# Performance work log

Measured on AMD Instinct MI355X. Metric: run time of the kernel, lower is better.

The kernel has to match this reference:

```python
import jax, jax.numpy as jnp
import numpy as np

WS = 16      # window_size
OWS = 24     # overlap_win_size = int(16*0.5) + 16
PAD = 4      # (OWS - WS) // 2
NH = 6       # num_heads
DIM = 192
MLP_HID = 384  # dim * mlp_ratio(2)
TABLE = (WS + OWS - 1) ** 2  # 1521


def _ln(x, g, b, eps=1e-5):
    m = x.mean(-1, keepdims=True)
    v = ((x - m) ** 2).mean(-1, keepdims=True)
    return (x - m) * jax.lax.rsqrt(v + eps) * g + b


def setup_inputs() -> dict:
    key = jax.random.key(0)
    ks = jax.random.split(key, 16)
    B, H, W, C = 1, 192, 192, DIM
    x = jax.random.normal(ks[0], (B, H * W, C), jnp.float32)
    rpi = jax.random.randint(ks[1], (WS * WS, OWS * OWS), 0, TABLE, dtype=jnp.int64)
    s = 0.02
    return {
        "x": x,
        "rpi": rpi,
        "h": H,
        "w": W,
        "norm1_g": jnp.ones((C,), jnp.float32),
        "norm1_b": jnp.zeros((C,), jnp.float32),
        "qkv_w": jax.random.normal(ks[2], (C, 3 * C), jnp.float32) * s,
        "qkv_b": jnp.zeros((3 * C,), jnp.float32),
        "rpb_table": jax.random.normal(ks[3], (TABLE, NH), jnp.float32) * s,
        "proj_w": jax.random.normal(ks[4], (C, C), jnp.float32) * s,
        "proj_b": jnp.zeros((C,), jnp.float32),
        "norm2_g": jnp.ones((C,), jnp.float32),
        "norm2_b": jnp.zeros((C,), jnp.float32),
        "fc1_w": jax.random.normal(ks[5], (C, MLP_HID), jnp.float32) * s,
        "fc1_b": jnp.zeros((MLP_HID,), jnp.float32),
        "fc2_w": jax.random.normal(ks[6], (MLP_HID, C), jnp.float32) * s,
        "fc2_b": jnp.zeros((C,), jnp.float32),
    }


def reference(x, rpi, h, w, norm1_g, norm1_b, qkv_w, qkv_b, rpb_table,
              proj_w, proj_b, norm2_g, norm2_b, fc1_w, fc1_b, fc2_w, fc2_b):
    B, L, C = x.shape
    d = C // NH
    scale = d ** -0.5
    nhw, nww = h // WS, w // WS
    nW = nhw * nww

    shortcut = x
    xn = _ln(x, norm1_g, norm1_b).reshape(B, h, w, C)
    qkv = xn @ qkv_w + qkv_b                       # (B, h, w, 3C)
    q, k, v = jnp.split(qkv, 3, axis=-1)

    # non-overlapping query windows: (B*nW, WS*WS, C)
    qw = q.reshape(B, nhw, WS, nww, WS, C).transpose(0, 1, 3, 2, 4, 5)
    qw = qw.reshape(B * nW, WS * WS, C)

    # overlapping key/value windows via padded gather (equiv. to nn.Unfold)
    ri = (jnp.arange(nhw) * WS)[:, None] + jnp.arange(OWS)[None, :]  # (nhw, OWS)
    ci = (jnp.arange(nww) * WS)[:, None] + jnp.arange(OWS)[None, :]  # (nww, OWS)

    def win(t):
        tp = jnp.pad(t, ((0, 0), (PAD, PAD), (PAD, PAD), (0, 0)))
        g = tp[:, ri[:, :, None, None], ci[None, None, :, :], :]     # (B,nhw,OWS,nww,OWS,C)
        return g.transpose(0, 1, 3, 2, 4, 5).reshape(B * nW, OWS * OWS, C)

    kw, vw = win(k), win(v)

    qh = qw.reshape(B * nW, WS * WS, NH, d).transpose(0, 2, 1, 3) * scale
    kh = kw.reshape(B * nW, OWS * OWS, NH, d).transpose(0, 2, 1, 3)
    vh = vw.reshape(B * nW, OWS * OWS, NH, d).transpose(0, 2, 1, 3)

    attn = jnp.einsum('bhqd,bhkd->bhqk', qh, kh)
    bias = rpb_table[rpi.reshape(-1)].reshape(WS * WS, OWS * OWS, NH)
    bias = bias.transpose(2, 0, 1)                 # (NH, nq, n)
    attn = jax.nn.softmax(attn + bias[None], axis=-1)
    out = jnp.einsum('bhqk,bhkd->bhqd', attn, vh)
    out = out.transpose(0, 2, 1, 3).reshape(B * nW, WS * WS, C)

    # window reverse
    xr = out.reshape(B, nhw, nww, WS, WS, C).transpose(0, 1, 3, 2, 4, 5)
    xr = xr.reshape(B, h * w, C)

    x2 = xr @ proj_w + proj_b + shortcut
    x3 = _ln(x2, norm2_g, norm2_b)
    mlp = jax.nn.gelu(x3 @ fc1_w + fc1_b, approximate=False) @ fc2_w + fc2_b
    return x2 + mlp
```

## Files before the change

kernel.cpp:

```cpp
#include <hip/hip_runtime.h>
#include <hip/hip_bf16.h>

#define NH 6
#define DIM 192
#define HW 192
#define M_TOK (HW*HW)
#define QSC 0.25503488f
#define L2E 1.4426950408889634f

typedef __attribute__((ext_vector_type(8))) __bf16 bf16x8;
typedef __attribute__((ext_vector_type(8))) short short8;
typedef __attribute__((ext_vector_type(4))) short s16x4;
typedef __attribute__((ext_vector_type(4))) float floatx4;

__device__ inline unsigned short f2bf(float f) {
    union { float f; unsigned int u; } v; v.f = f;
    unsigned int r = (v.u + 0x7FFFu + ((v.u >> 16) & 1u)) >> 16;
    return (unsigned short)r;
}
__device__ inline short f2bfh(float f) {
    __bf16 b = (__bf16)f;
    return __builtin_bit_cast(short, b);
}
__device__ inline float exp2fast(float x) {
#if __has_builtin(__builtin_amdgcn_exp2f)
    return __builtin_amdgcn_exp2f(x);
#else
    return exp2f(x);
#endif
}
__device__ inline floatx4 bf4f(s16x4 b) {
    floatx4 f;
    #pragma unroll
    for (int r = 0; r < 4; r++) {
        union { unsigned u; float f; } v;
        v.u = ((unsigned)(unsigned short)b[r]) << 16;
        f[r] = v.f;
    }
    return f;
}

__device__ inline floatx4 mfma16(short8 a, short8 b, floatx4 c) {
    return __builtin_amdgcn_mfma_f32_16x16x32_bf16(
        __builtin_bit_cast(bf16x8, a), __builtin_bit_cast(bf16x8, b), c, 0, 0, 0);
}

template <int OFF>
__device__ inline s16x4 tr16(unsigned addr) {
    s16x4 r;
    asm volatile("ds_read_b64_tr_b16 %0, %1 offset:%2"
                 : "=&v"(r) : "v"(addr), "i"(OFF));
    return r;
}
template <int OFF>
__device__ inline s16x4 tr16m(unsigned addr) {
    s16x4 r;
    asm volatile("ds_read_b64_tr_b16 %0, %1 offset:%2"
                 : "=&v"(r) : "v"(addr), "i"(OFF) : "memory");
    return r;
}
template <int N>
__device__ __forceinline__ void wait_lgkm() {
    asm volatile("s_waitcnt lgkmcnt(%0)" :: "i"(N) : "memory");
}
template <int N>
__device__ __forceinline__ void wait_vm() {
    asm volatile("s_waitcnt vmcnt(%0)" :: "i"(N) : "memory");
}
__device__ __forceinline__ void bar_raw() {
    asm volatile("s_barrier" ::: "memory");
}
__device__ inline short8 cat8(s16x4 a, s16x4 b) {
    return __builtin_shufflevector(a, b, 0, 1, 2, 3, 4, 5, 6, 7);
}

__device__ __forceinline__ void gload16(const void* g, unsigned lds_off) {
    __builtin_amdgcn_global_load_lds(
        (const __attribute__((address_space(1))) unsigned int*)(uintptr_t)g,
        (__attribute__((address_space(3))) unsigned int*)(uintptr_t)lds_off,
        16, 0, 0);
}

__device__ __forceinline__ void btfrag_body(int id, const int* __restrict__ rpi,
                                            const float* __restrict__ table,
                                            unsigned short* __restrict__ btf) {
    int lane = id & 63;
    int t = id >> 6;
    int kt = t % 36; t /= 36;
    int qt = t & 15; int hh = t >> 4;
    int k = kt * 16 + (lane & 15);
    int qb = qt * 16 + (lane >> 4) * 4;
    s16x4 v;
    #pragma unroll
    for (int r = 0; r < 4; r++)
        v[r] = f2bfh(table[rpi[(qb + r) * 576 + k] * NH + hh] * L2E);
    *(s16x4*)&btf[(size_t)id * 4] = v;
}

__device__ __forceinline__ void wcast_rest_body(int i2, const float* __restrict__ projw,
                                                const float* __restrict__ fc1w,
                                                const float* __restrict__ fc2w,
                                                unsigned short* __restrict__ wt_proj,
                                                unsigned short* __restrict__ wt_fc1,
                                                unsigned short* __restrict__ wt_fc2) {
    if (i2 < 36864) {
        int n = i2 / 192, k = i2 - n * 192;
        wt_proj[i2] = f2bf(projw[k * 192 + n]);
    } else if (i2 < 110592) {
        int i = i2 - 36864;
        int n = i / 192, k = i - n * 192;
        wt_fc1[i] = f2bf(fc1w[k * 384 + n]);
    } else {
        int i = i2 - 110592;
        int n = i / 384, k = i - n * 384;
        wt_fc2[i] = f2bf(fc2w[k * 192 + n]);
    }
}

__global__ __launch_bounds__(256) void prep_kernel(
    const float* __restrict__ qkvw,
    const float* __restrict__ x, const float* __restrict__ n1g,
    const float* __restrict__ n1b,
    unsigned short* __restrict__ wt_qkv,
    unsigned short* __restrict__ xn) {
    int bid = blockIdx.x;
    if (bid < 432) {
        int id = bid * 256 + threadIdx.x;
        int n = id / 192, k = id - n * 192;
        wt_qkv[id] = f2bf(qkvw[k * 576 + n]);
    } else {
        int row = (bid - 432) * 4 + (threadIdx.x >> 6);
        int lane = threadIdx.x & 63;
        const float* r = x + (size_t)row * DIM;
        float x0 = r[lane], x1 = r[lane + 64], x2 = r[lane + 128];
        float s = x0 + x1 + x2;
        #pragma unroll
        for (int m = 32; m >= 1; m >>= 1) s += __shfl_xor(s, m);
        float mean = s * (1.f / 192.f);
        float d0 = x0 - mean, d1 = x1 - mean, d2 = x2 - mean;
        float v = d0 * d0 + d1 * d1 + d2 * d2;
        #pragma unroll
        for (int m = 32; m >= 1; m >>= 1) v += __shfl_xor(v, m);
        float rstd = rsqrtf(v * (1.f / 192.f) + 1e-5f);
        unsigned short* o = xn + (size_t)row * DIM;
        o[lane]       = f2bf(d0 * rstd * n1g[lane]       + n1b[lane]);
        o[lane + 64]  = f2bf(d1 * rstd * n1g[lane + 64]  + n1b[lane + 64]);
        o[lane + 128] = f2bf(d2 * rstd * n1g[lane + 128] + n1b[lane + 128]);
    }
}

template <int MODE, int KK>
__global__ __launch_bounds__(256, 4) void gemm_kernel(
    const unsigned short* __restrict__ A,
    const unsigned short* __restrict__ Wt,
    const float* __restrict__ bias,
    void* __restrict__ outp,
    int N,
    const int* __restrict__ rpi, const float* __restrict__ table,
    unsigned short* __restrict__ btf,
    const float* __restrict__ projw, const float* __restrict__ fc1w,
    const float* __restrict__ fc2w,
    unsigned short* __restrict__ wt_proj, unsigned short* __restrict__ wt_fc1,
    unsigned short* __restrict__ wt_fc2) {
    if (MODE == 0 && blockIdx.y >= 9) {
        int extra = (blockIdx.y - 9) * 288 + blockIdx.x;
        if (extra < 864) {
            btfrag_body(extra * 256 + threadIdx.x, rpi, table, btf);
        } else if (extra < 1584) {
            wcast_rest_body((extra - 864) * 256 + threadIdx.x,
                            projw, fc1w, fc2w, wt_proj, wt_fc1, wt_fc2);
        }
        return;
    }
    __shared__ __align__(16) short sAB[19968];
    constexpr int STAGES = KK / 96;
    int tid = threadIdx.x;
    int w = tid >> 6, lane = tid & 63;
    int bm = blockIdx.x, bn = blockIdx.y;
    int lr = lane & 15, h = lane >> 4;
    floatx4 acc[2][4];
    #pragma unroll
    for (int i = 0; i < 2; i++)
        #pragma unroll
        for (int j = 0; j < 4; j++) acc[i][j] = (floatx4){0.f, 0.f, 0.f, 0.f};

    unsigned ldsbase = (unsigned)(uintptr_t)&sAB[0];

    for (int s = 0; s < STAGES; s++) {
        if (s) __syncthreads();
        for (int W = w; W < 39; W += 4) {
            int o = W * 1024 + lane * 16;
            const unsigned short* src;
            if (o < 26624) {
                int r = o / 208;
                int c = (o - r * 208) >> 4; c = c < 12 ? c : 11;
                src = &A[(size_t)(bm * 128 + r) * KK + s * 96 + c * 8];
            } else {
                int o2 = o - 26624;
                int r = o2 / 208;
                int c = (o2 - r * 208) >> 4; c = c < 12 ? c : 11;
                src = &Wt[(size_t)(bn * 64 + r) * KK + s * 96 + c * 8];
            }
            gload16(src, ldsbase + (unsigned)(W * 1024));
        }
        __syncthreads();
        #pragma unroll
        for (int kk = 0; kk < 3; kk++) {
            int kc = (kk * 4 + h) * 8;
            short8 a0 = *(const short8*)&sAB[(w * 32 + lr) * 104 + kc];
            short8 a1 = *(const short8*)&sAB[(w * 32 + 16 + lr) * 104 + kc];
            short8 b0 = *(const short8*)&sAB[13312 + (lr) * 104 + kc];
            short8 b1 = *(const short8*)&sAB[13312 + (16 + lr) * 104 + kc];
            short8 b2 = *(const short8*)&sAB[13312 + (32 + lr) * 104 + kc];
            short8 b3 = *(const short8*)&sAB[13312 + (48 + lr) * 104 + kc];
            acc[0][0] = mfma16(a0, b0, acc[0][0]);
            acc[0][1] = mfma16(a0, b1, acc[0][1]);
            acc[0][2] = mfma16(a0, b2, acc[0][2]);
            acc[0][3] = mfma16(a0, b3, acc[0][3]);
            acc[1][0] = mfma16(a1, b0, acc[1][0]);
            acc[1][1] = mfma16(a1, b1, acc[1][1]);
            acc[1][2] = mfma16(a1, b2, acc[1][2]);
            acc[1][3] = mfma16(a1, b3, acc[1][3]);
        }
    }

    int rowbase = bm * 128 + w * 32 + h * 4;
    int colbase = bn * 64;
    #pragma unroll
    for (int mi = 0; mi < 2; mi++) {
        #pragma unroll
        for (int ni = 0; ni < 4; ni++) {
            int c = colbase + ni * 16 + lr;
            float bv = bias[c];
            #pragma unroll
            for (int j = 0; j < 4; j++) {
                int r = rowbase + mi * 16 + j;
                float v = acc[mi][ni][j] + bv;
                if (MODE == 0) {
                    int part = c / 192;
                    int rem = c - part * 192;
                    int hd = rem >> 5, d = rem & 31;
                    if (part == 0) v *= QSC;
                    ((unsigned short*)outp)[((size_t)(part * 6 + hd) * M_TOK + r) * 32 + d] = f2bf(v);
                }
            }
        }
    }
}

__global__ __launch_bounds__(256, 3) void mega_kernel(
    const unsigned short* __restrict__ Aop,
    const unsigned short* __restrict__ Wp,
    const unsigned short* __restrict__ W1,
    const unsigned short* __restrict__ W2,
    const float* __restrict__ pb,
    const float* __restrict__ b1,
    const float* __restrict__ b2f,
    const float* __restrict__ res,
    const float* __restrict__ g2, const float* __restrict__ bb2,
    float* __restrict__ outp) {
    __shared__ __align__(16) short sA[13312];
    __shared__ __align__(16) short sH[4608];
    __shared__ __align__(16) short sB[6656];
    int tid = threadIdx.x;
    int w = tid >> 6, lane = tid & 63;
    int bm = blockIdx.x;
    int lr = lane & 15, h = lane >> 4;
    int lrow0 = w * 16 + h * 4;
    int row0 = bm * 64 + lrow0;

    floatx4 x2a[12];
    #pragma unroll
    for (int t = 0; t < 12; t++) x2a[t] = (floatx4){0.f, 0.f, 0.f, 0.f};

    short8 rg0, rg1, rg2;
    auto loadreg96 = [&](const unsigned short* base) {
        #pragma unroll
        for (int k = 0; k < 3; k++) {
            int d = (k * 256 + tid) * 16;
            int r = d / 192, cc = (d - r * 192) >> 1;
            short8 v = *(const short8*)&base[r * 192 + cc];
            if (k == 0) rg0 = v; else if (k == 1) rg1 = v; else rg2 = v;
        }
    };
    auto write96 = [&]() {
        #pragma unroll
        for (int k = 0; k < 3; k++) {
            int d = (k * 256 + tid) * 16;
            int r = d / 192, cc = (d - r * 192) >> 1;
            *(short8*)&sB[r * 104 + cc] = (k == 0) ? rg0 : (k == 1) ? rg1 : rg2;
        }
    };
    auto loadreg64 = [&](const unsigned short* base) {
        #pragma unroll
        for (int k = 0; k < 2; k++) {
            int d = (k * 256 + tid) * 16;
            int r = d / 128, cc = (d - r * 128) >> 1;
            short8 v = *(const short8*)&base[r * 384 + cc];
            if (k == 0) rg0 = v; else rg1 = v;
        }
    };
    auto write64 = [&]() {
        #pragma unroll
        for (int k = 0; k < 2; k++) {
            int d = (k * 256 + tid) * 16;
            int r = d / 128, cc = (d - r * 128) >> 1;
            *(short8*)&sB[r * 72 + cc] = (k == 0) ? rg0 : rg1;
        }
    };

    auto comp96 = [&](floatx4* acc, const short* Ap) {
        #pragma unroll
        for (int kk = 0; kk < 3; kk++) {
            int kc = (kk * 4 + h) * 8;
            short8 a = *(const short8*)&Ap[(w * 16 + lr) * 104 + kc];
            #pragma unroll
            for (int ni = 0; ni < 4; ni++) {
                short8 b = *(const short8*)&sB[(ni * 16 + lr) * 104 + kc];
                acc[ni] = mfma16(a, b, acc[ni]);
            }
        }
    };
    auto comp64 = [&](floatx4* acc) {
        #pragma unroll
        for (int kk = 0; kk < 2; kk++) {
            int kc = (kk * 4 + h) * 8;
            short8 a = *(const short8*)&sH[(w * 16 + lr) * 72 + kc];
            #pragma unroll
            for (int ni = 0; ni < 4; ni++) {
                short8 b = *(const short8*)&sB[(ni * 16 + lr) * 72 + kc];
                acc[ni] = mfma16(a, b, acc[ni]);
            }
        }
    };

#define SCH __builtin_amdgcn_sched_barrier(0)
#define ST96(LOADER, ACC, AP) \
    bar_raw(); wait_vm<0>(); SCH; write96(); LOADER; wait_lgkm<0>(); SCH; \
    bar_raw(); comp96(ACC, AP);
#define ST96F(LOADER, ACC, AP) \
    wait_vm<0>(); SCH; write96(); LOADER; wait_lgkm<0>(); SCH; \
    bar_raw(); comp96(ACC, AP);
#define ST64(LOADER, ACC) \
    bar_raw(); wait_vm<0>(); SCH; write64(); LOADER; wait_lgkm<0>(); SCH; \
    bar_raw(); comp64(ACC);

    {
        unsigned ldsA = (unsigned)(uintptr_t)&sA[0];
        for (int W = w; W < 26; W += 4) {
            int o = W * 1024 + lane * 16;
            int sl = o / 13312;
            int o2 = o - sl * 13312;
            int r = o2 / 208;
            int c = (o2 - r * 208) >> 4; c = c < 12 ? c : 11;
            int col = sl * 96 + c * 8;
            int hd = col >> 5, d = col & 31;
            gload16(&Aop[((size_t)hd * M_TOK + bm * 64 + r) * 32 + d],
                    ldsA + (unsigned)(W * 1024));
        }
    }
    loadreg96(Wp);

    ST96F(loadreg96(Wp + 64 * 192),        &x2a[0], sA);
    ST96(loadreg96(Wp + 128 * 192),        &x2a[4], sA);
    ST96(loadreg96(Wp + 96),               &x2a[8], sA);
    ST96(loadreg96(Wp + 64 * 192 + 96),    &x2a[0], sA + 6656);
    ST96(loadreg96(Wp + 128 * 192 + 96),   &x2a[4], sA + 6656);
    ST96(loadreg96(W1),                    &x2a[8], sA + 6656);

    {
        float s1[4] = {0.f, 0.f, 0.f, 0.f}, s2[4] = {0.f, 0.f, 0.f, 0.f};
        #pragma unroll
        for (int t = 0; t < 12; t++) {
            int c = t * 16 + lr;
            float bv = pb[c];
            #pragma unroll
            for (int j = 0; j < 4; j++) {
                size_t idx = (size_t)(row0 + j) * 192 + c;
                float v = x2a[t][j] + bv + res[idx];
                x2a[t][j] = v;
                s1[j] += v;
                s2[j] += v * v;
            }
        }
        #pragma unroll
        for (int mask = 1; mask <= 8; mask <<= 1) {
            #pragma unroll
            for (int j = 0; j < 4; j++) {
                s1[j] += __shfl_xor(s1[j], mask);
                s2[j] += __shfl_xor(s2[j], mask);
            }
        }
        float mean[4], rstd[4];
        #pragma unroll
        for (int j = 0; j < 4; j++) {
            mean[j] = s1[j] * (1.f / 192.f);
            float var = s2[j] * (1.f / 192.f) - mean[j] * mean[j];
            rstd[j] = rsqrtf(var + 1e-5f);
        }
        #pragma unroll
        for (int t = 0; t < 12; t++) {
            int c = t * 16 + lr;
            float gw = g2[c], bw = bb2[c];
            int slab = t / 6;
            int cc = c - slab * 96;
            #pragma unroll
            for (int j = 0; j < 4; j++) {
                float lnv = (x2a[t][j] - mean[j]) * rstd[j] * gw + bw;
                sA[slab * 6656 + (lrow0 + j) * 104 + cc] = f2bfh(lnv);
            }
        }
    }

    for (int hg = 0; hg < 6; hg++) {
        floatx4 ha[4];
        #pragma unroll
        for (int ni = 0; ni < 4; ni++) ha[ni] = (floatx4){0.f, 0.f, 0.f, 0.f};

        ST96(loadreg96(W1 + (size_t)(hg * 64) * 192 + 96), ha, sA);
        ST96(loadreg64(W2 + hg * 64),                      ha, sA + 6656);

        #pragma unroll
        for (int ni = 0; ni < 4; ni++) {
            int hc = hg * 64 + ni * 16 + lr;
            float bv = b1[hc];
            #pragma unroll
            for (int j = 0; j < 4; j++) {
                float v = ha[ni][j] + bv;
                float gl = 0.5f * v * (1.f + erff(v * 0.70710678118654752f));
                sH[(lrow0 + j) * 72 + ni * 16 + lr] = f2bfh(gl);
            }
        }

        ST64(loadreg64(W2 + (size_t)64 * 384 + hg * 64),  &x2a[0]);
        ST64(loadreg64(W2 + (size_t)128 * 384 + hg * 64), &x2a[4]);
        if (hg < 5) {
            ST64(loadreg96(W1 + (size_t)((hg + 1) * 64) * 192), &x2a[8]);
        } else {
            ST64(, &x2a[8]);
        }
    }
#undef ST96
#undef ST96F
#undef ST64
#undef SCH

    #pragma unroll
    for (int t = 0; t < 12; t++) {
        int c = t * 16 + lr;
        float bv = b2f[c];
        #pragma unroll
        for (int j = 0; j < 4; j++) {
            size_t idx = (size_t)(row0 + j) * 192 + c;
            outp[idx] = x2a[t][j] + bv;
        }
    }
}

__global__ __launch_bounds__(256, 3) void attn_mfma_kernel(
    const unsigned short* __restrict__ qkv,
    const unsigned short* __restrict__ btf,
    unsigned short* __restrict__ out) {
    __shared__ __align__(16) short sK[2][2304];
    __shared__ __align__(16) short sV[2][2048];
    __shared__ __align__(16) short sPt[4][4096];
    int win = blockIdx.x, head = blockIdx.y;
    int iy = win / 12, ix = win % 12;
    int tid = threadIdx.x;
    int w = tid >> 6, lane = tid & 63;
    int m = lane & 15, h = lane >> 4;

    const unsigned short* Qp = qkv + (size_t)head * M_TOK * 32;
    const unsigned short* Kp = qkv + (size_t)(6 + head) * M_TOK * 32;

    short8 qf[4];
    #pragma unroll
    for (int i = 0; i < 4; i++) {
        int wy = w * 4 + i;
        size_t tok = (size_t)(iy * 16 + wy) * HW + ix * 16 + m;
        qf[i] = *(const short8*)&Qp[tok * 32 + h * 8];
    }

    short ob = (m == 0) ? (short)0x3F80 : (short)0;
    short8 bones = {ob, ob, ob, ob, ob, ob, ob, ob};

    floatx4 oacc[4][2];
    floatx4 lacc[4];
    #pragma unroll
    for (int i = 0; i < 4; i++) {
        lacc[i] = (floatx4){0.f, 0.f, 0.f, 0.f};
        oacc[i][0] = (floatx4){0.f, 0.f, 0.f, 0.f};
        oacc[i][1] = (floatx4){0.f, 0.f, 0.f, 0.f};
    }

    int skey = tid >> 2, dq = tid & 3;
    short* kdst = &sK[0][skey * 36 + dq * 8];
    short* vdst = &sV[0][(dq >> 1) * 1024 + (skey >> 2) * 64 + (skey & 3) * 16 + (dq & 1) * 8];

    auto fetch = [&](int c, short8& kv, short8& vv) {
        int key = c * 64 + skey;
        int oy = key / 24, ox = key - (key / 24) * 24;
        int gy = iy * 16 - 4 + oy, gx = ix * 16 - 4 + ox;
        kv = (short8){0,0,0,0,0,0,0,0};
        vv = (short8){0,0,0,0,0,0,0,0};
        if (gy >= 0 && gy < HW && gx >= 0 && gx < HW) {
            const unsigned short* p = &Kp[((size_t)gy * HW + gx) * 32 + dq * 8];
            kv = *(const short8*)p;
            vv = *(const short8*)(p + 6 * M_TOK * 32);
        }
    };

    {
        short8 kv, vv;
        fetch(0, kv, vv);
        *(short8*)kdst = kv;
        *(short8*)vdst = vv;
    }

    unsigned sPbase = (unsigned)(uintptr_t)&sPt[w][0];
    unsigned sPa = sPbase + 8 * m + 256 * h;
    unsigned sVa0 = (unsigned)(uintptr_t)&sV[0][0] + 8 * m + 256 * h;
    char* sPwb = (char*)&sPt[w][0] + 128 * (m >> 2) + 32 * (m & 3) + 8 * h;

    for (int c = 0; c < 9; c++) {
        __syncthreads();
        int cur = c & 1;
        short8 knx, vnx;
        bool more = (c < 8);
        if (more) fetch(c + 1, knx, vnx);

        const short* sKc = sK[cur];
        short8 kfrag[4];
        #pragma unroll
        for (int kt = 0; kt < 4; kt++)
            kfrag[kt] = *(const short8*)&sKc[(kt * 16 + m) * 36 + h * 8];

        const unsigned short* bb = btf + ((((size_t)head * 16 + w * 4) * 36 + c * 4) * 64 + lane) * 4;

        #pragma unroll
        for (int i = 0; i < 4; i++) {
            floatx4 s[4];
            #pragma unroll
            for (int kt = 0; kt < 4; kt++)
                s[kt] = bf4f(*(const s16x4*)&bb[(size_t)(i * 36 + kt) * 256]);
            #pragma unroll
            for (int kt = 0; kt < 4; kt++)
                s[kt] = mfma16(qf[i], kfrag[kt], s[kt]);
            #pragma unroll
            for (int kt = 0; kt < 4; kt++) {
                s16x4 pk;
                #pragma unroll
                for (int r = 0; r < 4; r++)
                    pk[r] = f2bfh(exp2fast(s[kt][r]));
                *(s16x4*)(sPwb + i * 2048 + kt * 512) = pk;
            }
        }

        unsigned sVa = sVa0 + cur * 4096;
        short8 vb[4];
        {
            s16x4 lo0 = tr16<0>(sVa),    hi0 = tr16<128>(sVa);
            s16x4 lo1 = tr16<2048>(sVa), hi1 = tr16<2176>(sVa);
            s16x4 lo2 = tr16<1024>(sVa), hi2 = tr16<1152>(sVa);
            s16x4 lo3 = tr16<3072>(sVa), hi3 = tr16<3200>(sVa);
            vb[0] = cat8(lo0, hi0);
            vb[1] = cat8(lo1, hi1);
            vb[2] = cat8(lo2, hi2);
            vb[3] = cat8(lo3, hi3);
        }
        s16x4 pl0 = tr16m<0>(sPa),    ph0 = tr16m<128>(sPa);
        s16x4 pl1 = tr16m<1024>(sPa), ph1 = tr16m<1152>(sPa);
        #pragma unroll
        for (int i = 0; i < 4; i++) {
            s16x4 nl0, nh0, nl1, nh1;
            if (i < 3) {
                unsigned a = sPa + (unsigned)((i + 1) * 2048);
                nl0 = tr16m<0>(a);    nh0 = tr16m<128>(a);
                nl1 = tr16m<1024>(a); nh1 = tr16m<1152>(a);
                wait_lgkm<4>();
            } else {
                wait_lgkm<0>();
            }
            __builtin_amdgcn_sched_barrier(0);
            short8 pa0 = cat8(pl0, ph0);
            short8 pa1 = cat8(pl1, ph1);
            oacc[i][0] = mfma16(pa0, vb[0], oacc[i][0]);
            oacc[i][1] = mfma16(pa0, vb[1], oacc[i][1]);
            oacc[i][0] = mfma16(pa1, vb[2], oacc[i][0]);
            oacc[i][1] = mfma16(pa1, vb[3], oacc[i][1]);
            lacc[i] = mfma16(pa0, bones, lacc[i]);
            lacc[i] = mfma16(pa1, bones, lacc[i]);
            if (i < 3) { pl0 = nl0; ph0 = nh0; pl1 = nl1; ph1 = nh1; }
        }

        if (more) {
            int nb = 1 - cur;
            *(short8*)(kdst + nb * 2304) = knx;
            *(short8*)(vdst + nb * 2048) = vnx;
        }
    }

    unsigned short* Op = out + (size_t)head * M_TOK * 32;
    #pragma unroll
    for (int i = 0; i < 4; i++) {
        float inv[4];
        #pragma unroll
        for (int r = 0; r < 4; r++) {
            float sum = __shfl(lacc[i][r], lane & 48);
            inv[r] = 1.f / sum;
        }
        int wy = w * 4 + i;
        #pragma unroll
        for (int dt = 0; dt < 2; dt++)
            #pragma unroll
            for (int r = 0; r < 4; r++) {
                size_t tok = (size_t)(iy * 16 + wy) * HW + ix * 16 + h * 4 + r;
                Op[tok * 32 + dt * 16 + m] = f2bf(oacc[i][dt][r] * inv[r]);
            }
    }
}

extern "C" void kernel_launch(void* const* d_in, const int* in_sizes, int n_in,
                              void* d_out, int out_size, void* d_ws, size_t ws_size,
                              hipStream_t stream) {
    const float* x     = (const float*)d_in[0];
    const int*   rpi   = (const int*)d_in[1];
    const float* n1g   = (const float*)d_in[4];
    const float* n1b   = (const float*)d_in[5];
    const float* qkvw  = (const float*)d_in[6];
    const float* qkvb  = (const float*)d_in[7];
    const float* rpb   = (const float*)d_in[8];
    const float* projw = (const float*)d_in[9];
    const float* projb = (const float*)d_in[10];
    const float* n2g   = (const float*)d_in[11];
    const float* n2b   = (const float*)d_in[12];
    const float* fc1w  = (const float*)d_in[13];
    const float* fc1b  = (const float*)d_in[14];
    const float* fc2w  = (const float*)d_in[15];
    const float* fc2b  = (const float*)d_in[16];

    char* ws = (char*)d_ws;
    unsigned short* wt_qkv  = (unsigned short*)ws;
    unsigned short* wt_proj = wt_qkv + 110592;
    unsigned short* wt_fc1  = wt_proj + 36864;
    unsigned short* wt_fc2  = wt_fc1 + 73728;
    unsigned short* btf     = (unsigned short*)(ws + 589824);
    unsigned short* xn      = (unsigned short*)(ws + 4128768);
    unsigned short* qkv     = (unsigned short*)(ws + 18284544);
    unsigned short* attn_o  = (unsigned short*)(ws + 60751872);

    prep_kernel<<<9648, 256, 0, stream>>>(qkvw, x, n1g, n1b, wt_qkv, xn);
    gemm_kernel<0, 192><<<dim3(288, 15), 256, 0, stream>>>(
        xn, wt_qkv, qkvb, qkv, 576,
        rpi, rpb, btf, projw, fc1w, fc2w, wt_proj, wt_fc1, wt_fc2);
    attn_mfma_kernel<<<dim3(144, 6), 256, 0, stream>>>(qkv, btf, attn_o);
    mega_kernel<<<576, 256, 0, stream>>>(
        attn_o, wt_proj, wt_fc1, wt_fc2, projb, fc1b, fc2b,
        x, n2g, n2b, (float*)d_out);
}
```

Measured before the change: 130.6 us.

## Restructure QKV GEMM to keep A tile resident and stream weight tiles

```diff
diff --git a/kernel.cpp b/kernel.cpp
--- a/kernel.cpp
+++ b/kernel.cpp
@@ -149,21 +149,20 @@
     }
 }
 
-template <int MODE, int KK>
-__global__ __launch_bounds__(256, 4) void gemm_kernel(
+__global__ __launch_bounds__(256, 3) void qkv_kernel(
     const unsigned short* __restrict__ A,
     const unsigned short* __restrict__ Wt,
     const float* __restrict__ bias,
-    void* __restrict__ outp,
-    int N,
+    unsigned short* __restrict__ outp,
     const int* __restrict__ rpi, const float* __restrict__ table,
     unsigned short* __restrict__ btf,
     const float* __restrict__ projw, const float* __restrict__ fc1w,
     const float* __restrict__ fc2w,
     unsigned short* __restrict__ wt_proj, unsigned short* __restrict__ wt_fc1,
     unsigned short* __restrict__ wt_fc2) {
-    if (MODE == 0 && blockIdx.y >= 9) {
-        int extra = (blockIdx.y - 9) * 288 + blockIdx.x;
+    int bx = blockIdx.x;
+    if (bx >= 576) {
+        int extra = bx - 576;
         if (extra < 864) {
             btfrag_body(extra * 256 + threadIdx.x, rpi, table, btf);
         } else if (extra < 1584) {
@@ -172,77 +171,92 @@
         }
         return;
     }
-    __shared__ __align__(16) short sAB[19968];
-    constexpr int STAGES = KK / 96;
+    __shared__ __align__(16) short sA[13312];
+    __shared__ __align__(16) short sB[6656];
     int tid = threadIdx.x;
     int w = tid >> 6, lane = tid & 63;
-    int bm = blockIdx.x, bn = blockIdx.y;
+    int bm = bx;
     int lr = lane & 15, h = lane >> 4;
-    floatx4 acc[2][4];
-    #pragma unroll
-    for (int i = 0; i < 2; i++)
-        #pragma unroll
-        for (int j = 0; j < 4; j++) acc[i][j] = (floatx4){0.f, 0.f, 0.f, 0.f};
-
-    unsigned ldsbase = (unsigned)(uintptr_t)&sAB[0];
-
-    for (int s = 0; s < STAGES; s++) {
-        if (s) __syncthreads();
-        for (int W = w; W < 39; W += 4) {
+
+    short8 rg0, rg1, rg2;
+    auto loadreg96 = [&](const unsigned short* base) {
+        #pragma unroll
+        for (int k = 0; k < 3; k++) {
+            int d = (k * 256 + tid) * 16;
+            int r = d / 192, cc = (d - r * 192) >> 1;
+            short8 v = *(const short8*)&base[r * 192 + cc];
+            if (k == 0) rg0 = v; else if (k == 1) rg1 = v; else rg2 = v;
+        }
+    };
+    auto write96 = [&]() {
+        #pragma unroll
+        for (int k = 0; k < 3; k++) {
+            int d = (k * 256 + tid) * 16;
+            int r = d / 192, cc = (d - r * 192) >> 1;
+            *(short8*)&sB[r * 104 + cc] = (k == 0) ? rg0 : (k == 1) ? rg1 : rg2;
+        }
+    };
+
+    {
+        unsigned ldsA = (unsigned)(uintptr_t)&sA[0];
+        for (int W = w; W < 26; W += 4) {
             int o = W * 1024 + lane * 16;
-            const unsigned short* src;
-            if (o < 26624) {
-                int r = o / 208;
-                int c = (o - r * 208) >> 4; c = c < 12 ? c : 11;
-                src = &A[(size_t)(bm * 128 + r) * KK + s * 96 + c * 8];
-            } else {
-                int o2 = o - 26624;
-                int r = o2 / 208;
-                int c = (o2 - r * 208) >> 4; c = c < 12 ? c : 11;
-                src = &Wt[(size_t)(bn * 64 + r) * KK + s * 96 + c * 8];
-            }
-            gload16(src, ldsbase + (unsigned)(W * 1024));
-        }
-        __syncthreads();
-        #pragma unroll
-        for (int kk = 0; kk < 3; kk++) {
-            int kc = (kk * 4 + h) * 8;
-            short8 a0 = *(const short8*)&sAB[(w * 32 + lr) * 104 + kc];
-            short8 a1 = *(const short8*)&sAB[(w * 32 + 16 + lr) * 104 + kc];
-            short8 b0 = *(const short8*)&sAB[13312 + (lr) * 104 + kc];
-            short8 b1 = *(const short8*)&sAB[13312 + (16 + lr) * 104 + kc];
-            short8 b2 = *(const short8*)&sAB[13312 + (32 + lr) * 104 + kc];
-            short8 b3 = *(const short8*)&sAB[13312 + (48 + lr) * 104 + kc];
-            acc[0][0] = mfma16(a0, b0, acc[0][0]);
-            acc[0][1] = mfma16(a0, b1, acc[0][1]);
-            acc[0][2] = mfma16(a0, b2, acc[0][2]);
-            acc[0][3] = mfma16(a0, b3, acc[0][3]);
-            acc[1][0] = mfma16(a1, b0, acc[1][0]);
-            acc[1][1] = mfma16(a1, b1, acc[1][1]);
-            acc[1][2] = mfma16(a1, b2, acc[1][2]);
-            acc[1][3] = mfma16(a1, b3, acc[1][3]);
-        }
-    }
-
-    int rowbase = bm * 128 + w * 32 + h * 4;
-    int colbase = bn * 64;
-    #pragma unroll
-    for (int mi = 0; mi < 2; mi++) {
+            int sl = o / 13312;
+            int o2 = o - sl * 13312;
+            int r = o2 / 208;
+            int c = (o2 - r * 208) >> 4; c = c < 12 ? c : 11;
+            int col = sl * 96 + c * 8;
+            gload16(&A[(size_t)(bm * 64 + r) * 192 + col],
+                    ldsA + (unsigned)(W * 1024));
+        }
+    }
+    loadreg96(Wt);
+
+    int rowbase = bm * 64 + w * 16 + h * 4;
+    for (int bn = 0; bn < 9; bn++) {
+        floatx4 acc[4];
+        #pragma unroll
+        for (int ni = 0; ni < 4; ni++) acc[ni] = (floatx4){0.f, 0.f, 0.f, 0.f};
+
+        #pragma unroll
+        for (int ks = 0; ks < 2; ks++) {
+            int s = bn * 2 + ks;
+            bar_raw();
+            wait_vm<0>();
+            __builtin_amdgcn_sched_barrier(0);
+            write96();
+            if (s < 17) {
+                int ns = s + 1;
+                loadreg96(Wt + (size_t)((ns >> 1) * 64) * 192 + (ns & 1) * 96);
+            }
+            wait_lgkm<0>();
+            __builtin_amdgcn_sched_barrier(0);
+            bar_raw();
+            const short* Ap = sA + ks * 6656;
+            #pragma unroll
+            for (int kk = 0; kk < 3; kk++) {
+                int kc = (kk * 4 + h) * 8;
+                short8 a = *(const short8*)&Ap[(w * 16 + lr) * 104 + kc];
+                #pragma unroll
+                for (int ni = 0; ni < 4; ni++) {
+                    short8 b = *(const short8*)&sB[(ni * 16 + lr) * 104 + kc];
+                    acc[ni] = mfma16(a, b, acc[ni]);
+                }
+            }
+        }
+
         #pragma unroll
         for (int ni = 0; ni < 4; ni++) {
-            int c = colbase + ni * 16 + lr;
+            int c = bn * 64 + ni * 16 + lr;
             float bv = bias[c];
+            int part = c / 192;
+            int rem = c - part * 192;
+            int hd = rem >> 5, d = rem & 31;
             #pragma unroll
             for (int j = 0; j < 4; j++) {
-                int r = rowbase + mi * 16 + j;
-                float v = acc[mi][ni][j] + bv;
-                if (MODE == 0) {
-                    int part = c / 192;
-                    int rem = c - part * 192;
-                    int hd = rem >> 5, d = rem & 31;
-                    if (part == 0) v *= QSC;
-                    ((unsigned short*)outp)[((size_t)(part * 6 + hd) * M_TOK + r) * 32 + d] = f2bf(v);
-                }
+                float v = acc[ni][j] + bv;
+                if (part == 0) v *= QSC;
+                outp[((size_t)(part * 6 + hd) * M_TOK + rowbase + j) * 32 + d] = f2bf(v);
             }
         }
     }
@@ -650,8 +664,8 @@
     unsigned short* attn_o  = (unsigned short*)(ws + 60751872);
 
     prep_kernel<<<9648, 256, 0, stream>>>(qkvw, x, n1g, n1b, wt_qkv, xn);
-    gemm_kernel<0, 192><<<dim3(288, 15), 256, 0, stream>>>(
-        xn, wt_qkv, qkvb, qkv, 576,
+    qkv_kernel<<<2160, 256, 0, stream>>>(
+        xn, wt_qkv, qkvb, qkv,
         rpi, rpb, btf, projw, fc1w, fc2w, wt_proj, wt_fc1, wt_fc2);
     attn_mfma_kernel<<<dim3(144, 6), 256, 0, stream>>>(qkv, btf, attn_o);
     mega_kernel<<<576, 256, 0, stream>>>(
```

Result: slower. 136.3 us (+4.4%).
